# Kernel optimization log

Hardware: AMD Instinct MI355X
Metric: run time of the kernel (lower is better)

The kernel has to match this reference:

```python
import jax, jax.numpy as jnp
import numpy as np

WINDOW_SIZE = 11
SIGMA = 1.5
DATA_RANGE = 1.0
CHANNEL = 3
K1 = 0.01
K2 = 0.03
EPS = 1e-08


def _gaussian_window(window_size, sigma, channel):
    # 1D gaussian normalized to sum 1, then outer product -> 2D window
    xs = np.arange(window_size) - window_size // 2
    g = np.exp(-(xs.astype(np.float32) ** 2) / (2.0 * sigma ** 2))
    g = g / g.sum()
    w2d = np.outer(g, g).astype(np.float32)  # [K, K]
    # depthwise kernel in OIHW layout: [channel, 1, K, K]
    return jnp.asarray(np.broadcast_to(w2d, (channel, 1, window_size, window_size)))


def _depthwise_blur(img, window):
    # img: [B, C, H, W], window: [C, 1, K, K]; SAME padding depthwise conv
    pad = WINDOW_SIZE // 2
    return jax.lax.conv_general_dilated(
        img, window,
        window_strides=(1, 1),
        padding=[(pad, pad), (pad, pad)],
        dimension_numbers=("NCHW", "OIHW", "NCHW"),
        feature_group_count=CHANNEL,
    )


def setup_inputs() -> dict:
    key = jax.random.key(0)
    kx, ky = jax.random.split(key)
    x = jax.random.uniform(kx, (32, 3, 512, 512), dtype=jnp.float32)
    y = jax.random.uniform(ky, (32, 3, 512, 512), dtype=jnp.float32)
    return {"x": x, "y": y}


def reference(x, y):
    window = _gaussian_window(WINDOW_SIZE, SIGMA, CHANNEL)
    C1 = (K1 * DATA_RANGE) ** 2
    C2 = (K2 * DATA_RANGE) ** 2

    mu_x = _depthwise_blur(x, window)
    mu_y = _depthwise_blur(y, window)
    mu_x2 = mu_x * mu_x
    mu_y2 = mu_y * mu_y
    mu_xy = mu_x * mu_y

    sigma_x2 = _depthwise_blur(x * x, window) - mu_x2
    sigma_y2 = _depthwise_blur(y * y, window) - mu_y2
    sigma_xy = _depthwise_blur(x * y, window) - mu_xy

    num = (2.0 * mu_xy + C1) * (2.0 * sigma_xy + C2)
    den = (mu_x2 + mu_y2 + C1) * (sigma_x2 + sigma_y2 + C2)
    ssim_map = num / (den + EPS)
    return 1.0 - jnp.mean(ssim_map)
```

## Files before the change

### kernel.cpp

```cpp
#include <hip/hip_runtime.h>

typedef float v4f   __attribute__((ext_vector_type(4)));
typedef float f32x4 __attribute__((ext_vector_type(4)));
typedef _Float16 h4 __attribute__((ext_vector_type(4)));
typedef _Float16 h8 __attribute__((ext_vector_type(8)));

#define HH 512
#define WW 512
#define NPLANES 96
#define NSTRIP 32
#define NBLK (NPLANES * NSTRIP)
#define C1V 1e-4f
#define C2V 9e-4f
#define EPSV 1e-8f
#define NPIX 25165824.0f

#define SLOT_B 784
#define Q_B    3920
#define LDS_B  19600

#define MF(A, B) __builtin_amdgcn_mfma_f32_16x16x32_f16((A), (B), zf, 0, 0, 0)

#define SELW(DST, IX) { const int ix_ = (IX); float r_ = 0.f; \
  r_ = (ix_ == 0) ? wv0 : r_;  r_ = (ix_ == 1) ? wv1 : r_; \
  r_ = (ix_ == 2) ? wv2 : r_;  r_ = (ix_ == 3) ? wv3 : r_; \
  r_ = (ix_ == 4) ? wv4 : r_;  r_ = (ix_ == 5) ? wv5 : r_; \
  r_ = (ix_ == 6) ? wv6 : r_;  r_ = (ix_ == 7) ? wv7 : r_; \
  r_ = (ix_ == 8) ? wv8 : r_;  r_ = (ix_ == 9) ? wv9 : r_; \
  r_ = (ix_ == 10) ? wv10 : r_; DST = r_; }

#define PACK8(DST, F0,F1,F2,F3,F4,F5,F6,F7) \
  DST = (h8){(_Float16)(F0),(_Float16)(F1),(_Float16)(F2),(_Float16)(F3), \
             (_Float16)(F4),(_Float16)(F5),(_Float16)(F6),(_Float16)(F7)};

#define EPX(M) { \
  const float mux_ = mx[M], muy_ = my[M]; \
  const float mx2_ = mux_ * mux_, my2_ = muy_ * muy_, mxy_ = mux_ * muy_; \
  const float sx2_ = vx2[M] - mx2_, sy2_ = vy2[M] - my2_, sxy_ = vxy[M] - mxy_; \
  const float num_ = fmaf(2.f, mxy_, C1V) * fmaf(2.f, sxy_, C2V); \
  const float den_ = (mx2_ + my2_ + C1V) * (sx2_ + sy2_ + C2V) + EPSV; \
  acc = fmaf(num_, __builtin_amdgcn_rcpf(den_), acc); }

#define VLOAD(TAU) { \
  const int tau_ = (TAU); \
  const int ch_ = tau_ - 1 + ((s + 1) >> 1); \
  const int slot_ = ((unsigned)ch_ < 32u) ? (ch_ & 3) : 4; \
  const char* rb_ = lds + slot_ * SLOT_B + rByte; \
  vbx  = *(const h8*)(rb_); \
  vby  = *(const h8*)(rb_ + Q_B); \
  vbx2 = *(const h8*)(rb_ + 2 * Q_B); \
  vby2 = *(const h8*)(rb_ + 3 * Q_B); \
  vbxy = *(const h8*)(rb_ + 4 * Q_B); }

#define VMFMA { \
  const f32x4 mx  = MF(Wf, vbx);  const f32x4 my  = MF(Wf, vby); \
  const f32x4 vx2 = MF(Wf, vbx2); const f32x4 vy2 = MF(Wf, vby2); \
  const f32x4 vxy = MF(Wf, vbxy); \
  EPX(0) EPX(1) EPX(2) EPX(3) }

#define STEP(T, CXA,CXB,CYA,CYB, NXA,NXB,NYA,NYB) { \
  const int t_ = (T); \
  if (t_ >= 2) VLOAD(t_ - 2) \
  if (t_ < 31) { \
    NXA = *(const v4f*)pXa; NXB = *(const v4f*)pXb; \
    NYA = *(const v4f*)pYa; NYB = *(const v4f*)pYb; \
    pXa += 16 * WW; pXb += 16 * WW; pYa += 16 * WW; pYb += 16 * WW; \
  } \
  h8 ax, ay; \
  PACK8(ax, CXA[0],CXA[1],CXA[2],CXA[3], CXB[0],CXB[1],CXB[2],CXB[3]) \
  PACK8(ay, CYA[0],CYA[1],CYA[2],CYA[3], CYB[0],CYB[1],CYB[2],CYB[3]) \
  const h8 ax2 = ax * ax, ay2 = ay * ay, axy = ax * ay; \
  const f32x4 chx  = MF(ax,  WfH); const f32x4 chy  = MF(ay,  WfH); \
  const f32x4 chx2 = MF(ax2, WfH); const f32x4 chy2 = MF(ay2, WfH); \
  const f32x4 chxy = MF(axy, WfH); \
  { char* wb_ = lds + (t_ & 3) * SLOT_B + wByte; \
    *(h4*)(wb_)         = (h4){(_Float16)chx[0], (_Float16)chx[1], (_Float16)chx[2], (_Float16)chx[3]}; \
    *(h4*)(wb_ + Q_B)   = (h4){(_Float16)chy[0], (_Float16)chy[1], (_Float16)chy[2], (_Float16)chy[3]}; \
    *(h4*)(wb_ + 2*Q_B) = (h4){(_Float16)chx2[0],(_Float16)chx2[1],(_Float16)chx2[2],(_Float16)chx2[3]}; \
    *(h4*)(wb_ + 3*Q_B) = (h4){(_Float16)chy2[0],(_Float16)chy2[1],(_Float16)chy2[2],(_Float16)chy2[3]}; \
    *(h4*)(wb_ + 4*Q_B) = (h4){(_Float16)chxy[0],(_Float16)chxy[1],(_Float16)chxy[2],(_Float16)chxy[3]}; } \
  if (t_ >= 2) VMFMA }

__global__ __launch_bounds__(64)
void ssim_main(const float* __restrict__ x, const float* __restrict__ y,
               float* __restrict__ partial)
{
  __shared__ __attribute__((aligned(16))) char lds[LDS_B];

  const int l = threadIdx.x;
  const int n = l & 15;
  const int s = l >> 4;

  const int wg = blockIdx.x;
  const int swz = (wg & 7) * (NBLK / 8) + (wg >> 3);
  const int plane = swz >> 5;
  const int strip = swz & 31;
  const int C0 = strip * 16;

  const float* xp = x + (size_t)plane * (HH * WW);
  const float* yp = y + (size_t)plane * (HH * WW);

  float wv0, wv1, wv2, wv3, wv4, wv5, wv6, wv7, wv8, wv9, wv10;
#define WINIT(k) wv##k = expf(-((float)((k - 5) * (k - 5))) / 4.5f);
  WINIT(0) WINIT(1) WINIT(2) WINIT(3) WINIT(4) WINIT(5)
  WINIT(6) WINIT(7) WINIT(8) WINIT(9) WINIT(10)
#undef WINIT
  const float inv_ = 1.f / (wv0 + wv1 + wv2 + wv3 + wv4 + wv5 + wv6 + wv7 + wv8 + wv9 + wv10);
#define WNORM(k) wv##k = __int_as_float(__builtin_amdgcn_readfirstlane(__float_as_int(wv##k * inv_)));
  WNORM(0) WNORM(1) WNORM(2) WNORM(3) WNORM(4) WNORM(5)
  WNORM(6) WNORM(7) WNORM(8) WNORM(9) WNORM(10)
#undef WNORM

  const f32x4 zf = {0.f, 0.f, 0.f, 0.f};

  h8 Wf;
  {
    const int kb = 8 * s;
    float b0,b1,b2,b3,b4,b5,b6,b7;
    SELW(b0, kb + 0 - n - 3) SELW(b1, kb + 1 - n - 3)
    SELW(b2, kb + 2 - n - 3) SELW(b3, kb + 3 - n - 3)
    SELW(b4, kb + 4 - n - 3) SELW(b5, kb + 5 - n - 3)
    SELW(b6, kb + 6 - n - 3) SELW(b7, kb + 7 - n - 3)
    PACK8(Wf, b0,b1,b2,b3,b4,b5,b6,b7)
  }

  const int cb = C0 - 8 + 8 * s;
  const bool kill = (cb < 0) || (cb >= WW);
  h8 WfH = Wf;
  if (kill) WfH = (h8)(_Float16)0.f;
  const int ca = kill ? 0 : cb;

  const float* pXa = xp + n * WW + ca;
  const float* pXb = pXa + 4;
  const float* pYa = yp + n * WW + ca;
  const float* pYb = pYa + 4;

  const int wByte = n * 48 + 8 * s;
  const int rByte = n * 48 + 16 * ((s + 1) & 1);

  #pragma unroll
  for (int q = 0; q < 5; ++q)
    #pragma unroll
    for (int j = 0; j < 3; ++j)
      *(unsigned*)(lds + q * Q_B + 4 * SLOT_B + 4 * (l + 64 * j)) = 0u;

  h8 vbx, vby, vbx2, vby2, vbxy;
  float acc = 0.f;

  v4f XA0 = *(const v4f*)pXa, XB0 = *(const v4f*)pXb;
  v4f YA0 = *(const v4f*)pYa, YB0 = *(const v4f*)pYb;
  pXa += 16 * WW; pXb += 16 * WW; pYa += 16 * WW; pYb += 16 * WW;
  v4f XA1, XB1, YA1, YB1;

  #pragma unroll 1
  for (int u = 0; u < 16; ++u) {
    STEP(2 * u,     XA0, XB0, YA0, YB0,  XA1, XB1, YA1, YB1)
    STEP(2 * u + 1, XA1, XB1, YA1, YB1,  XA0, XB0, YA0, YB0)
  }
  VLOAD(30) VMFMA
  VLOAD(31) VMFMA

  #pragma unroll
  for (int off = 32; off > 0; off >>= 1) acc += __shfl_down(acc, off);
  if (l == 0) partial[wg] = acc;
}

__global__ void finalize_kernel(const float* __restrict__ partial, float* __restrict__ out)
{
  __shared__ float s4[4];
  float a = 0.f;
  for (int i = threadIdx.x; i < NBLK; i += 256) a += partial[i];
  #pragma unroll
  for (int off = 32; off > 0; off >>= 1) a += __shfl_down(a, off);
  if ((threadIdx.x & 63) == 0) s4[threadIdx.x >> 6] = a;
  __syncthreads();
  if (threadIdx.x == 0) out[0] = 1.f - (s4[0] + s4[1] + s4[2] + s4[3]) * (1.f / NPIX);
}

extern "C" void kernel_launch(void* const* d_in, const int* in_sizes, int n_in,
                              void* d_out, int out_size, void* d_ws, size_t ws_size,
                              hipStream_t stream)
{
  const float* x = (const float*)d_in[0];
  const float* y = (const float*)d_in[1];
  float* ws = (float*)d_ws;
  float* out = (float*)d_out;

  hipLaunchKernelGGL(ssim_main, dim3(NBLK), dim3(64), 0, stream, x, y, ws);
  hipLaunchKernelGGL(finalize_kernel, dim3(1), dim3(256), 0, stream, ws, out);
}
```

Measured before the change: 66.11 us.

## Split each column strip into two row halves with halo and deeper prefetch

Each workgroup now handles half the rows of a 16-column strip, which doubles the grid to 6144 single-wave blocks. Each half recomputes a one-chunk halo above and below, with out-of-range rows handled by masking the weights instead of a zero LDS slot. Global loads are prefetched two chunks ahead instead of one, and the LDS footprint shrinks. The goal is more parallelism and latency hiding, at the cost of redundant halo row work (18 chunks per 16 computed) and more blocks to schedule.

```diff
diff --git a/kernel.cpp b/kernel.cpp
--- a/kernel.cpp
+++ b/kernel.cpp
@@ -9,15 +9,16 @@
 #define WW 512
 #define NPLANES 96
 #define NSTRIP 32
-#define NBLK (NPLANES * NSTRIP)
+#define NHALF 2
+#define NBLK (NPLANES * NSTRIP * NHALF)
 #define C1V 1e-4f
 #define C2V 9e-4f
 #define EPSV 1e-8f
 #define NPIX 25165824.0f
 
 #define SLOT_B 784
-#define Q_B    3920
-#define LDS_B  19600
+#define Q_B    3136
+#define LDS_B  15680
 
 #define MF(A, B) __builtin_amdgcn_mfma_f32_16x16x32_f16((A), (B), zf, 0, 0, 0)
 
@@ -41,11 +42,9 @@
   const float den_ = (mx2_ + my2_ + C1V) * (sx2_ + sy2_ + C2V) + EPSV; \
   acc = fmaf(num_, __builtin_amdgcn_rcpf(den_), acc); }
 
-#define VLOAD(TAU) { \
-  const int tau_ = (TAU); \
-  const int ch_ = tau_ - 1 + ((s + 1) >> 1); \
-  const int slot_ = ((unsigned)ch_ < 32u) ? (ch_ & 3) : 4; \
-  const char* rb_ = lds + slot_ * SLOT_B + rByte; \
+#define VLOADL(O) { \
+  const int c_ = (O) + ((s + 1) >> 1); \
+  const char* rb_ = lds + (c_ & 3) * SLOT_B + rByte; \
   vbx  = *(const h8*)(rb_); \
   vby  = *(const h8*)(rb_ + Q_B); \
   vbx2 = *(const h8*)(rb_ + 2 * Q_B); \
@@ -58,28 +57,32 @@
   const f32x4 vxy = MF(Wf, vbxy); \
   EPX(0) EPX(1) EPX(2) EPX(3) }
 
-#define STEP(T, CXA,CXB,CYA,CYB, NXA,NXB,NYA,NYB) { \
+#define STEP(T, CXA,CXB,CYA,CYB) { \
   const int t_ = (T); \
-  if (t_ >= 2) VLOAD(t_ - 2) \
-  if (t_ < 31) { \
-    NXA = *(const v4f*)pXa; NXB = *(const v4f*)pXb; \
-    NYA = *(const v4f*)pYa; NYB = *(const v4f*)pYb; \
-    pXa += 16 * WW; pXb += 16 * WW; pYa += 16 * WW; pYb += 16 * WW; \
-  } \
+  if (t_ >= 3) VLOADL(t_ - 3) \
   h8 ax, ay; \
   PACK8(ax, CXA[0],CXA[1],CXA[2],CXA[3], CXB[0],CXB[1],CXB[2],CXB[3]) \
   PACK8(ay, CYA[0],CYA[1],CYA[2],CYA[3], CYB[0],CYB[1],CYB[2],CYB[3]) \
+  if (t_ + 2 < 18) { \
+    const int rb2_ = min(max((Gbase + t_ + 2) * 16, 0), 496); \
+    const float* qx_ = xp + (size_t)rb2_ * WW; \
+    const float* qy_ = yp + (size_t)rb2_ * WW; \
+    CXA = *(const v4f*)(qx_ + offA); CXB = *(const v4f*)(qx_ + offB); \
+    CYA = *(const v4f*)(qy_ + offA); CYB = *(const v4f*)(qy_ + offB); \
+  } \
+  const bool rOK_ = (unsigned)(Gbase + t_) < 32u; \
+  const h8 wfh_ = rOK_ ? WfH : (h8)(_Float16)0.f; \
   const h8 ax2 = ax * ax, ay2 = ay * ay, axy = ax * ay; \
-  const f32x4 chx  = MF(ax,  WfH); const f32x4 chy  = MF(ay,  WfH); \
-  const f32x4 chx2 = MF(ax2, WfH); const f32x4 chy2 = MF(ay2, WfH); \
-  const f32x4 chxy = MF(axy, WfH); \
+  const f32x4 chx  = MF(ax,  wfh_); const f32x4 chy  = MF(ay,  wfh_); \
+  const f32x4 chx2 = MF(ax2, wfh_); const f32x4 chy2 = MF(ay2, wfh_); \
+  const f32x4 chxy = MF(axy, wfh_); \
   { char* wb_ = lds + (t_ & 3) * SLOT_B + wByte; \
     *(h4*)(wb_)         = (h4){(_Float16)chx[0], (_Float16)chx[1], (_Float16)chx[2], (_Float16)chx[3]}; \
     *(h4*)(wb_ + Q_B)   = (h4){(_Float16)chy[0], (_Float16)chy[1], (_Float16)chy[2], (_Float16)chy[3]}; \
     *(h4*)(wb_ + 2*Q_B) = (h4){(_Float16)chx2[0],(_Float16)chx2[1],(_Float16)chx2[2],(_Float16)chx2[3]}; \
     *(h4*)(wb_ + 3*Q_B) = (h4){(_Float16)chy2[0],(_Float16)chy2[1],(_Float16)chy2[2],(_Float16)chy2[3]}; \
     *(h4*)(wb_ + 4*Q_B) = (h4){(_Float16)chxy[0],(_Float16)chxy[1],(_Float16)chxy[2],(_Float16)chxy[3]}; } \
-  if (t_ >= 2) VMFMA }
+  if (t_ >= 3) VMFMA }
 
 __global__ __launch_bounds__(64)
 void ssim_main(const float* __restrict__ x, const float* __restrict__ y,
@@ -93,9 +96,12 @@
 
   const int wg = blockIdx.x;
   const int swz = (wg & 7) * (NBLK / 8) + (wg >> 3);
-  const int plane = swz >> 5;
-  const int strip = swz & 31;
+  const int plane = swz >> 6;
+  const int rem = swz & 63;
+  const int strip = rem & 31;
+  const int half = rem >> 5;
   const int C0 = strip * 16;
+  const int Gbase = 16 * half - 1;
 
   const float* xp = x + (size_t)plane * (HH * WW);
   const float* yp = y + (size_t)plane * (HH * WW);
@@ -130,35 +136,35 @@
   if (kill) WfH = (h8)(_Float16)0.f;
   const int ca = kill ? 0 : cb;
 
-  const float* pXa = xp + n * WW + ca;
-  const float* pXb = pXa + 4;
-  const float* pYa = yp + n * WW + ca;
-  const float* pYb = pYa + 4;
+  const int offA = n * WW + ca;
+  const int offB = offA + 4;
 
   const int wByte = n * 48 + 8 * s;
   const int rByte = n * 48 + 16 * ((s + 1) & 1);
 
-  #pragma unroll
-  for (int q = 0; q < 5; ++q)
-    #pragma unroll
-    for (int j = 0; j < 3; ++j)
-      *(unsigned*)(lds + q * Q_B + 4 * SLOT_B + 4 * (l + 64 * j)) = 0u;
-
   h8 vbx, vby, vbx2, vby2, vbxy;
   float acc = 0.f;
 
-  v4f XA0 = *(const v4f*)pXa, XB0 = *(const v4f*)pXb;
-  v4f YA0 = *(const v4f*)pYa, YB0 = *(const v4f*)pYb;
-  pXa += 16 * WW; pXb += 16 * WW; pYa += 16 * WW; pYb += 16 * WW;
-  v4f XA1, XB1, YA1, YB1;
+  v4f XA0, XB0, YA0, YB0, XA1, XB1, YA1, YB1;
+  {
+    const int rb0 = min(max(Gbase * 16, 0), 496);
+    const int rb1 = min(max((Gbase + 1) * 16, 0), 496);
+    const float* q0x = xp + (size_t)rb0 * WW;
+    const float* q0y = yp + (size_t)rb0 * WW;
+    const float* q1x = xp + (size_t)rb1 * WW;
+    const float* q1y = yp + (size_t)rb1 * WW;
+    XA0 = *(const v4f*)(q0x + offA); XB0 = *(const v4f*)(q0x + offB);
+    YA0 = *(const v4f*)(q0y + offA); YB0 = *(const v4f*)(q0y + offB);
+    XA1 = *(const v4f*)(q1x + offA); XB1 = *(const v4f*)(q1x + offB);
+    YA1 = *(const v4f*)(q1y + offA); YB1 = *(const v4f*)(q1y + offB);
+  }
 
   #pragma unroll 1
-  for (int u = 0; u < 16; ++u) {
-    STEP(2 * u,     XA0, XB0, YA0, YB0,  XA1, XB1, YA1, YB1)
-    STEP(2 * u + 1, XA1, XB1, YA1, YB1,  XA0, XB0, YA0, YB0)
+  for (int u = 0; u < 9; ++u) {
+    STEP(2 * u,     XA0, XB0, YA0, YB0)
+    STEP(2 * u + 1, XA1, XB1, YA1, YB1)
   }
-  VLOAD(30) VMFMA
-  VLOAD(31) VMFMA
+  VLOADL(15) VMFMA
 
   #pragma unroll
   for (int off = 32; off > 0; off >>= 1) acc += __shfl_down(acc, off);
```

Measured after the change: 69.90 us. +5.7%, slower.
